# Optimization experiments

Measured on AMD Instinct MI355X. Metric: run time of the kernel, lower is better.

Reference implementation:

```python
import jax, jax.numpy as jnp
import numpy as np

DIM, KEY_DIM, HEADS, RATIO, RES = 384, 32, 8, 4, 7
N = RES * RES
D = RATIO * KEY_DIM          # 128 per-head value dim
DH = D * HEADS               # 1024
NHKD = KEY_DIM * HEADS       # 256
SCALE = KEY_DIM ** -0.5


def _make_bias_idxs(res):
    points = [(i, j) for i in range(res) for j in range(res)]
    offsets = {}
    idxs = []
    for p1 in points:
        for p2 in points:
            off = (abs(p1[0] - p2[0]), abs(p1[1] - p2[1]))
            if off not in offsets:
                offsets[off] = len(offsets)
            idxs.append(offsets[off])
    n = len(points)
    return np.asarray(idxs, dtype=np.int32).reshape(n, n), len(offsets)


def setup_inputs() -> dict:
    key = jax.random.key(0)
    ks = jax.random.split(key, 10)
    B = 2048
    idxs_np, n_off = _make_bias_idxs(RES)
    s = 0.02
    return {
        "x": jax.random.normal(ks[0], (B, N, DIM), jnp.float32),
        "q_w": jax.random.normal(ks[1], (NHKD, DIM), jnp.float32) * s,
        "q_b": jnp.zeros((NHKD,), jnp.float32),
        "k_w": jax.random.normal(ks[2], (NHKD, DIM), jnp.float32) * s,
        "k_b": jnp.zeros((NHKD,), jnp.float32),
        "v_w": jax.random.normal(ks[3], (DH, DIM), jnp.float32) * s,
        "v_b": jnp.zeros((DH,), jnp.float32),
        "proj_w": jax.random.normal(ks[4], (DIM, DH), jnp.float32) * s,
        "proj_b": jnp.zeros((DIM,), jnp.float32),
        "attention_biases": jax.random.normal(ks[5], (HEADS, n_off), jnp.float32) * s,
        "bias_idxs": jnp.asarray(idxs_np),  # [N, N] int32
    }


def reference(x, q_w, q_b, k_w, k_b, v_w, v_b, proj_w, proj_b,
              attention_biases, bias_idxs):
    B, n, _ = x.shape
    q = (x @ q_w.T + q_b).reshape(B, n, HEADS, KEY_DIM)
    k = (x @ k_w.T + k_b).reshape(B, n, HEADS, KEY_DIM)
    v = (x @ v_w.T + v_b).reshape(B, n, HEADS, D)
    # learned relative-position bias gathered per (query, key) pair: [H, N, N]
    ab = attention_biases[:, bias_idxs]
    attn = jnp.einsum("bnhd,bmhd->bhnm", q, k) * SCALE + ab
    attn = jax.nn.softmax(attn, axis=-1)
    out = jnp.einsum("bhnm,bmhd->bnhd", attn, v).reshape(B, n, DH)
    return out @ proj_w.T + proj_b
```

## Files before the change

### kernel.cpp

```cpp
#include <hip/hip_runtime.h>
#include <hip/hip_bf16.h>

#define NTOK   49
#define DIM    384
#define KEY_DIM 32
#define HEADS  8
#define D_HEAD 128
#define SCALE  0.17677669529663687f

typedef short short8 __attribute__((ext_vector_type(8)));
typedef short short4_t __attribute__((ext_vector_type(4)));
typedef float f32x4 __attribute__((ext_vector_type(4)));

__device__ __forceinline__ unsigned short f2bf(float x) {
    union { float f; unsigned u; } v; v.f = x;
    unsigned r = v.u + 0x7fffu + ((v.u >> 16) & 1u);
    return (unsigned short)(r >> 16);
}

__device__ __forceinline__ f32x4 MFMA(short8 a, short8 b, f32x4 c) {
    return __builtin_amdgcn_mfma_f32_16x16x32_bf16(a, b, c, 0, 0, 0);
}

__global__ void prologue(const float* __restrict__ qw, const float* __restrict__ qb,
                         const float* __restrict__ kw,
                         const float* __restrict__ vw, const float* __restrict__ pw,
                         const float* __restrict__ biases, const int* __restrict__ idxs,
                         int n_off,
                         unsigned short* __restrict__ qk_p,
                         unsigned short* __restrict__ vw_p,
                         unsigned short* __restrict__ pw_p,
                         float* __restrict__ qb_s,
                         float* __restrict__ ab_t) {
    int t = blockIdx.x * 256 + threadIdx.x;
    if (t < 24576) {
        int lane = t & 63, kt = (t >> 6) % 12, ntile = t / 768;
        int c = ntile * 16 + (lane & 15), kk = kt * 32 + (lane >> 4) * 8;
        const float* src = (c < 256) ? (qw + c * 384 + kk) : (kw + (c - 256) * 384 + kk);
        float sc = (c < 256) ? SCALE : 1.0f;
        short8 o;
#pragma unroll
        for (int j = 0; j < 8; ++j) o[j] = (short)f2bf(src[j] * sc);
        *(short8*)(qk_p + (size_t)t * 8) = o;
    } else if (t < 73728) {
        int u = t - 24576;
        int lane = u & 63, kt = (u >> 6) % 12, ntile = u / 768;
        int c = ntile * 16 + (lane & 15), kk = kt * 32 + (lane >> 4) * 8;
        const float* src = vw + c * 384 + kk;
        short8 o;
#pragma unroll
        for (int j = 0; j < 8; ++j) o[j] = (short)f2bf(src[j]);
        *(short8*)(vw_p + (size_t)u * 8) = o;
    } else if (t < 122880) {
        int u = t - 73728;
        int lane = u & 63, kt = (u >> 6) % 32, ntile = u / 2048;
        int c = ntile * 16 + (lane & 15), kk = kt * 32 + (lane >> 4) * 8;
        const float* src = pw + c * 1024 + kk;
        short8 o;
#pragma unroll
        for (int j = 0; j < 8; ++j) o[j] = (short)f2bf(src[j]);
        *(short8*)(pw_p + (size_t)u * 8) = o;
    } else if (t < 123136) {
        int u = t - 122880;
        qb_s[u] = qb[u] * SCALE;
    } else if (t < 123136 + 32768) {
        int u = t - 123136;
        int h = u >> 12, n = (u >> 6) & 63, m = u & 63;
        float v = 0.f;
        if (m < 49 && n < 49) v = biases[h * n_off + idxs[n * 49 + m]];
        ab_t[u] = v;
    }
}

__global__ __launch_bounds__(512) void fused_attn(
        const float* __restrict__ x,
        const unsigned short* __restrict__ qkw,
        const unsigned short* __restrict__ vw,
        const unsigned short* __restrict__ pw,
        const float* __restrict__ qb_s, const float* __restrict__ kb,
        const float* __restrict__ vb, const float* __restrict__ pb,
        const float* __restrict__ ab_t,
        float* __restrict__ out) {

    __shared__ __align__(16) unsigned short smem[40656];
    unsigned short* xs  = smem;
    unsigned short* ps  = smem + 19208;
    unsigned short* vsT = smem + 22736;
    unsigned short* qs  = smem + 31952;
    unsigned short* ks2 = smem + 31952 + 2560;
    unsigned short* osA = smem + 31952;

    const int tid  = threadIdx.x;
    const int lane = tid & 63;
    const int wid  = tid >> 6;
    const int l15  = lane & 15;
    const int lg   = lane >> 4;
    const int b    = blockIdx.x;

    const float* xb = x + (size_t)b * (NTOK * DIM);
#pragma unroll 2
    for (int i = tid; i < 4704; i += 512) {
        f32x4 v = __builtin_nontemporal_load(((const f32x4*)xb) + i);
        int f = i * 4;
        int row = f / DIM;
        int col = f - row * DIM;
        short4_t pk;
        pk[0] = (short)f2bf(v[0]); pk[1] = (short)f2bf(v[1]);
        pk[2] = (short)f2bf(v[2]); pk[3] = (short)f2bf(v[3]);
        *(short4_t*)&xs[row * 392 + col] = pk;
    }
    __syncthreads();

    f32x4 pacc[3][4];
#pragma unroll
    for (int i = 0; i < 3; ++i)
#pragma unroll
        for (int j = 0; j < 4; ++j) pacc[i][j] = (f32x4)0.f;

    const f32x4 zf = (f32x4)0.f;

    for (int h = 0; h < HEADS; ++h) {
        {
            const int mh  = wid >> 2;
            const int nt0 = 3 * (wid & 3);
            const int rA0 = min(mh * 32 + l15, 48);
            const int rA1 = min(mh * 32 + 16 + l15, 48);
            f32x4 acc[3][2];
#pragma unroll
            for (int i = 0; i < 3; ++i) { acc[i][0] = zf; acc[i][1] = zf; }

            const short8* bptr[3];
#pragma unroll
            for (int i = 0; i < 3; ++i) {
                int nt = nt0 + i;
                const unsigned short* base; int ntile;
                if (nt < 2)      { base = qkw; ntile = 2 * h + nt; }
                else if (nt < 4) { base = qkw; ntile = 16 + 2 * h + (nt - 2); }
                else             { base = vw;  ntile = 8 * h + (nt - 4); }
                bptr[i] = (const short8*)(base + (size_t)ntile * 12 * 64 * 8);
            }
#pragma unroll
            for (int kt = 0; kt < 12; ++kt) {
                short8 a0 = *(const short8*)&xs[rA0 * 392 + kt * 32 + lg * 8];
                short8 a1 = *(const short8*)&xs[rA1 * 392 + kt * 32 + lg * 8];
#pragma unroll
                for (int i = 0; i < 3; ++i) {
                    short8 bf = bptr[i][kt * 64 + lane];
                    acc[i][0] = MFMA(a0, bf, acc[i][0]);
                    acc[i][1] = MFMA(a1, bf, acc[i][1]);
                }
            }
#pragma unroll
            for (int i = 0; i < 3; ++i) {
                int nt = nt0 + i;
                int c  = nt * 16 + l15;
                if (nt < 4) {
                    int cc = (nt < 2) ? c : c - 32;
                    float bias = (nt < 2) ? qb_s[h * 32 + cc] : kb[h * 32 + cc];
                    unsigned short* dst = (nt < 2) ? qs : ks2;
#pragma unroll
                    for (int j = 0; j < 2; ++j) {
                        int r0 = mh * 32 + j * 16 + lg * 4;
                        f32x4 v = acc[i][j];
#pragma unroll
                        for (int r = 0; r < 4; ++r)
                            dst[(r0 + r) * 40 + cc] = f2bf(v[r] + bias);
                    }
                } else {
                    int d = c - 64;
                    float bias = vb[h * 128 + d];
#pragma unroll
                    for (int j = 0; j < 2; ++j) {
                        int m0 = mh * 32 + j * 16 + lg * 4;
                        f32x4 v = acc[i][j];
                        short4_t pk;
#pragma unroll
                        for (int r = 0; r < 4; ++r) pk[r] = (short)f2bf(v[r] + bias);
                        *(short4_t*)&vsT[d * 72 + m0] = pk;
                    }
                }
            }
        }
        __syncthreads();

        if (wid < 4) {
            const int I = wid;
            const int rq = min(I * 16 + l15, 48);
            short8 bq = *(const short8*)&qs[rq * 40 + lg * 8];
            f32x4 s[4];
#pragma unroll
            for (int J = 0; J < 4; ++J) {
                short8 ak = *(const short8*)&ks2[(J * 16 + l15) * 40 + lg * 8];
                s[J] = MFMA(ak, bq, zf);
            }
            const f32x4* abn = (const f32x4*)(ab_t + ((h * 64 + I * 16 + l15) * 64));
            float sv[16];
            float mx = -1e30f;
#pragma unroll
            for (int J = 0; J < 4; ++J) {
                f32x4 a4 = abn[J * 4 + lg];
#pragma unroll
                for (int r = 0; r < 4; ++r) {
                    int m = J * 16 + lg * 4 + r;
                    float val = s[J][r] + a4[r];
                    if (m >= 49) val = -1e30f;
                    sv[J * 4 + r] = val;
                    mx = fmaxf(mx, val);
                }
            }
            mx = fmaxf(mx, __shfl_xor(mx, 16));
            mx = fmaxf(mx, __shfl_xor(mx, 32));
            float sum = 0.f;
#pragma unroll
            for (int t = 0; t < 16; ++t) { float e = __expf(sv[t] - mx); sv[t] = e; sum += e; }
            sum += __shfl_xor(sum, 16);
            sum += __shfl_xor(sum, 32);
            float inv = 1.0f / sum;
            int n = I * 16 + l15;
            if (n < 49) {
#pragma unroll
                for (int J = 0; J < 4; ++J)
#pragma unroll
                    for (int r = 0; r < 4; ++r) {
                        int m = J * 16 + lg * 4 + r;
                        ps[n * 72 + m] = f2bf(sv[J * 4 + r] * inv);
                    }
            }
        }
        __syncthreads();

        {
            const int np = wid >> 2;
            const int dp = wid & 3;
            const int rp0 = min(np * 32 + l15, 48);
            const int rp1 = min(np * 32 + 16 + l15, 48);
            f32x4 a00 = zf, a01 = zf, a10 = zf, a11 = zf;
#pragma unroll
            for (int kk = 0; kk < 2; ++kk) {
                short8 a0 = *(const short8*)&ps[rp0 * 72 + kk * 32 + lg * 8];
                short8 a1 = *(const short8*)&ps[rp1 * 72 + kk * 32 + lg * 8];
                short8 b0 = *(const short8*)&vsT[(dp * 32 + l15) * 72 + kk * 32 + lg * 8];
                short8 b1 = *(const short8*)&vsT[(dp * 32 + 16 + l15) * 72 + kk * 32 + lg * 8];
                a00 = MFMA(a0, b0, a00); a01 = MFMA(a0, b1, a01);
                a10 = MFMA(a1, b0, a10); a11 = MFMA(a1, b1, a11);
            }
            f32x4 accs[2][2] = {{a00, a01}, {a10, a11}};
#pragma unroll
            for (int jn = 0; jn < 2; ++jn)
#pragma unroll
                for (int jd = 0; jd < 2; ++jd) {
                    int r0 = np * 32 + jn * 16 + lg * 4;
                    int d0 = dp * 32 + jd * 16 + l15;
                    f32x4 v = accs[jn][jd];
#pragma unroll
                    for (int r = 0; r < 4; ++r) osA[(r0 + r) * 136 + d0] = f2bf(v[r]);
                }
        }
        __syncthreads();

        {
            const int nt0 = 3 * wid;
#pragma unroll
            for (int kt = 0; kt < 4; ++kt) {
                short8 a[4];
#pragma unroll
                for (int mi = 0; mi < 4; ++mi)
                    a[mi] = *(const short8*)&osA[(mi * 16 + l15) * 136 + kt * 32 + lg * 8];
#pragma unroll
                for (int i = 0; i < 3; ++i) {
                    short8 bf = ((const short8*)pw)[((size_t)(nt0 + i) * 32 + (h * 4 + kt)) * 64 + lane];
#pragma unroll
                    for (int mi = 0; mi < 4; ++mi)
                        pacc[i][mi] = MFMA(a[mi], bf, pacc[i][mi]);
                }
            }
        }
        __syncthreads();
    }

    float* ob = out + (size_t)b * (NTOK * 384);
#pragma unroll
    for (int i = 0; i < 3; ++i) {
        int c = (3 * wid + i) * 16 + l15;
        float bias = pb[c];
#pragma unroll
        for (int mi = 0; mi < 4; ++mi) {
            f32x4 v = pacc[i][mi];
#pragma unroll
            for (int r = 0; r < 4; ++r) {
                int n = mi * 16 + lg * 4 + r;
                if (n < 49) __builtin_nontemporal_store(v[r] + bias, &ob[n * 384 + c]);
            }
        }
    }
}

extern "C" void kernel_launch(void* const* d_in, const int* in_sizes, int n_in,
                              void* d_out, int out_size, void* d_ws, size_t ws_size,
                              hipStream_t stream) {
    const float* x      = (const float*)d_in[0];
    const float* qw     = (const float*)d_in[1];
    const float* qb     = (const float*)d_in[2];
    const float* kw     = (const float*)d_in[3];
    const float* kb     = (const float*)d_in[4];
    const float* vw     = (const float*)d_in[5];
    const float* vb     = (const float*)d_in[6];
    const float* pw     = (const float*)d_in[7];
    const float* pb     = (const float*)d_in[8];
    const float* biases = (const float*)d_in[9];
    const int*   idxs   = (const int*)d_in[10];
    int n_off = in_sizes[9] / HEADS;

    char* ws = (char*)d_ws;
    unsigned short* qk_p = (unsigned short*)ws;
    unsigned short* vw_p = (unsigned short*)(ws + 393216);
    unsigned short* pw_p = (unsigned short*)(ws + 1179648);
    float*          qb_s = (float*)(ws + 1966080);
    float*          ab_t = (float*)(ws + 1967104);

    prologue<<<609, 256, 0, stream>>>(qw, qb, kw, vw, pw, biases, idxs, n_off,
                                      qk_p, vw_p, pw_p, qb_s, ab_t);
    fused_attn<<<2048, 512, 0, stream>>>(x, qk_p, vw_p, pw_p, qb_s, kb, vb, pb,
                                         ab_t, (float*)d_out);
}
```

Before: 453.6 us.

## Split fused attention into QKV-attention kernel and separate output projection kernel

Splits the single fused kernel into two. attn_qkv computes per-head QKV projections, softmax and P·V, then writes bf16 per-head outputs in MFMA fragment layout to a workspace buffer. out_proj reads them back and applies the projection with a full register accumulator. The aim is to cut LDS use and register pressure so more blocks fit per CU (launch_bounds 512,4). The cost is roughly 268 MB of extra global traffic for the intermediate, and the split only runs when the workspace is large enough.

Result: slower. 478.3 us (+5.4%).

```diff
diff --git a/kernel.cpp b/kernel.cpp
--- a/kernel.cpp
+++ b/kernel.cpp
@@ -72,6 +72,256 @@
     }
 }
 
+__global__ __launch_bounds__(512, 4) void attn_qkv(
+        const float* __restrict__ x,
+        const unsigned short* __restrict__ qkw,
+        const unsigned short* __restrict__ vw,
+        const float* __restrict__ qb_s, const float* __restrict__ kb,
+        const float* __restrict__ vb,
+        const float* __restrict__ ab_t,
+        unsigned short* __restrict__ O_p) {
+
+    __shared__ __align__(16) unsigned short smem[37072];
+    unsigned short* xs  = smem;
+    unsigned short* ps  = smem + 19208;
+    unsigned short* vsT = smem + 22736;
+    unsigned short* qs  = smem + 31952;
+    unsigned short* ks2 = smem + 34512;
+
+    const int tid  = threadIdx.x;
+    const int lane = tid & 63;
+    const int wid  = tid >> 6;
+    const int l15  = lane & 15;
+    const int lg   = lane >> 4;
+    const int b    = blockIdx.x;
+
+    const float* xb = x + (size_t)b * (NTOK * DIM);
+#pragma unroll 2
+    for (int i = tid; i < 4704; i += 512) {
+        f32x4 v = __builtin_nontemporal_load(((const f32x4*)xb) + i);
+        int f = i * 4;
+        int row = f / DIM;
+        int col = f - row * DIM;
+        short4_t pk;
+        pk[0] = (short)f2bf(v[0]); pk[1] = (short)f2bf(v[1]);
+        pk[2] = (short)f2bf(v[2]); pk[3] = (short)f2bf(v[3]);
+        *(short4_t*)&xs[row * 392 + col] = pk;
+    }
+    __syncthreads();
+
+    const f32x4 zf = (f32x4)0.f;
+
+    for (int h = 0; h < HEADS; ++h) {
+        {
+            const int mh  = wid >> 2;
+            const int nt0 = 3 * (wid & 3);
+            const int rA0 = min(mh * 32 + l15, 48);
+            const int rA1 = min(mh * 32 + 16 + l15, 48);
+            f32x4 acc[3][2];
+#pragma unroll
+            for (int i = 0; i < 3; ++i) { acc[i][0] = zf; acc[i][1] = zf; }
+
+            const short8* bptr[3];
+#pragma unroll
+            for (int i = 0; i < 3; ++i) {
+                int nt = nt0 + i;
+                const unsigned short* base; int ntile;
+                if (nt < 2)      { base = qkw; ntile = 2 * h + nt; }
+                else if (nt < 4) { base = qkw; ntile = 16 + 2 * h + (nt - 2); }
+                else             { base = vw;  ntile = 8 * h + (nt - 4); }
+                bptr[i] = (const short8*)(base + (size_t)ntile * 12 * 64 * 8);
+            }
+#pragma unroll
+            for (int kt = 0; kt < 12; ++kt) {
+                short8 a0 = *(const short8*)&xs[rA0 * 392 + kt * 32 + lg * 8];
+                short8 a1 = *(const short8*)&xs[rA1 * 392 + kt * 32 + lg * 8];
+#pragma unroll
+                for (int i = 0; i < 3; ++i) {
+                    short8 bf = bptr[i][kt * 64 + lane];
+                    acc[i][0] = MFMA(a0, bf, acc[i][0]);
+                    acc[i][1] = MFMA(a1, bf, acc[i][1]);
+                }
+            }
+#pragma unroll
+            for (int i = 0; i < 3; ++i) {
+                int nt = nt0 + i;
+                int c  = nt * 16 + l15;
+                if (nt < 4) {
+                    int cc = (nt < 2) ? c : c - 32;
+                    float bias = (nt < 2) ? qb_s[h * 32 + cc] : kb[h * 32 + cc];
+                    unsigned short* dst = (nt < 2) ? qs : ks2;
+#pragma unroll
+                    for (int j = 0; j < 2; ++j) {
+                        int r0 = mh * 32 + j * 16 + lg * 4;
+                        f32x4 v = acc[i][j];
+#pragma unroll
+                        for (int r = 0; r < 4; ++r)
+                            dst[(r0 + r) * 40 + cc] = f2bf(v[r] + bias);
+                    }
+                } else {
+                    int d = c - 64;
+                    float bias = vb[h * 128 + d];
+#pragma unroll
+                    for (int j = 0; j < 2; ++j) {
+                        int m0 = mh * 32 + j * 16 + lg * 4;
+                        f32x4 v = acc[i][j];
+                        short4_t pk;
+#pragma unroll
+                        for (int r = 0; r < 4; ++r) pk[r] = (short)f2bf(v[r] + bias);
+                        *(short4_t*)&vsT[d * 72 + m0] = pk;
+                    }
+                }
+            }
+        }
+        __syncthreads();
+
+        if (wid < 4) {
+            const int I = wid;
+            const int rq = min(I * 16 + l15, 48);
+            short8 bq = *(const short8*)&qs[rq * 40 + lg * 8];
+            f32x4 s[4];
+#pragma unroll
+            for (int J = 0; J < 4; ++J) {
+                short8 ak = *(const short8*)&ks2[(J * 16 + l15) * 40 + lg * 8];
+                s[J] = MFMA(ak, bq, zf);
+            }
+            const f32x4* abn = (const f32x4*)(ab_t + ((h * 64 + I * 16 + l15) * 64));
+            float sv[16];
+            float mx = -1e30f;
+#pragma unroll
+            for (int J = 0; J < 4; ++J) {
+                f32x4 a4 = abn[J * 4 + lg];
+#pragma unroll
+                for (int r = 0; r < 4; ++r) {
+                    int m = J * 16 + lg * 4 + r;
+                    float val = s[J][r] + a4[r];
+                    if (m >= 49) val = -1e30f;
+                    sv[J * 4 + r] = val;
+                    mx = fmaxf(mx, val);
+                }
+            }
+            mx = fmaxf(mx, __shfl_xor(mx, 16));
+            mx = fmaxf(mx, __shfl_xor(mx, 32));
+            float sum = 0.f;
+#pragma unroll
+            for (int t = 0; t < 16; ++t) { float e = __expf(sv[t] - mx); sv[t] = e; sum += e; }
+            sum += __shfl_xor(sum, 16);
+            sum += __shfl_xor(sum, 32);
+            float inv = 1.0f / sum;
+            int n = I * 16 + l15;
+            if (n < 49) {
+#pragma unroll
+                for (int J = 0; J < 4; ++J)
+#pragma unroll
+                    for (int r = 0; r < 4; ++r) {
+                        int m = J * 16 + lg * 4 + r;
+                        ps[n * 72 + m] = f2bf(sv[J * 4 + r] * inv);
+                    }
+            }
+        }
+        __syncthreads();
+
+        {
+            const int np = wid >> 2;
+            const int dp = wid & 3;
+            const int rp0 = min(np * 32 + l15, 48);
+            const int rp1 = min(np * 32 + 16 + l15, 48);
+            f32x4 a00 = zf, a01 = zf, a10 = zf, a11 = zf;
+#pragma unroll
+            for (int kk = 0; kk < 2; ++kk) {
+                short8 a0 = *(const short8*)&ps[rp0 * 72 + kk * 32 + lg * 8];
+                short8 a1 = *(const short8*)&ps[rp1 * 72 + kk * 32 + lg * 8];
+                short8 b0 = *(const short8*)&vsT[(dp * 32 + l15) * 72 + kk * 32 + lg * 8];
+                short8 b1 = *(const short8*)&vsT[(dp * 32 + 16 + l15) * 72 + kk * 32 + lg * 8];
+                a00 = MFMA(a0, b0, a00); a01 = MFMA(a0, b1, a01);
+                a10 = MFMA(a1, b0, a10); a11 = MFMA(a1, b1, a11);
+            }
+            f32x4 accs[2][2] = {{a00, a01}, {a10, a11}};
+            unsigned short* ob = O_p + (((size_t)b * 8 + h) * 32) * 256;
+#pragma unroll
+            for (int jn = 0; jn < 2; ++jn)
+#pragma unroll
+                for (int jd = 0; jd < 2; ++jd) {
+                    int frag = (np * 2 + jn) * 8 + (dp * 2 + jd);
+                    f32x4 v = accs[jn][jd];
+                    short4_t pk;
+#pragma unroll
+                    for (int r = 0; r < 4; ++r) pk[r] = (short)f2bf(v[r]);
+                    __builtin_nontemporal_store(pk, (short4_t*)(ob + frag * 256 + lane * 4));
+                }
+        }
+        __syncthreads();
+    }
+}
+
+__global__ __launch_bounds__(256) void out_proj(
+        const unsigned short* __restrict__ O_p,
+        const unsigned short* __restrict__ pw,
+        const float* __restrict__ pb,
+        float* __restrict__ out) {
+
+    __shared__ __align__(16) unsigned short osB[64 * 136];
+
+    const int tid  = threadIdx.x;
+    const int lane = tid & 63;
+    const int wid  = tid >> 6;
+    const int l15  = lane & 15;
+    const int lg   = lane >> 4;
+    const int b    = blockIdx.x;
+
+    f32x4 acc[6][4];
+#pragma unroll
+    for (int i = 0; i < 6; ++i)
+#pragma unroll
+        for (int j = 0; j < 4; ++j) acc[i][j] = (f32x4)0.f;
+
+    for (int h = 0; h < HEADS; ++h) {
+        const unsigned short* ob = O_p + (((size_t)b * 8 + h) * 32) * 256;
+#pragma unroll
+        for (int s = tid; s < 2048; s += 256) {
+            int frag = s >> 6, ln = s & 63;
+            short4_t v = __builtin_nontemporal_load((const short4_t*)(ob + frag * 256 + ln * 4));
+            int mt = frag >> 3, dt = frag & 7;
+            int r0 = mt * 16 + ((ln >> 4) << 2), c = dt * 16 + (ln & 15);
+#pragma unroll
+            for (int r = 0; r < 4; ++r) osB[(r0 + r) * 136 + c] = v[r];
+        }
+        __syncthreads();
+
+#pragma unroll
+        for (int kt = 0; kt < 4; ++kt) {
+            short8 a[4];
+#pragma unroll
+            for (int mt = 0; mt < 4; ++mt)
+                a[mt] = *(const short8*)&osB[(mt * 16 + l15) * 136 + kt * 32 + lg * 8];
+#pragma unroll
+            for (int i = 0; i < 6; ++i) {
+                short8 bf = ((const short8*)pw)[((size_t)(wid * 6 + i) * 32 + (h * 4 + kt)) * 64 + lane];
+#pragma unroll
+                for (int mt = 0; mt < 4; ++mt)
+                    acc[i][mt] = MFMA(a[mt], bf, acc[i][mt]);
+            }
+        }
+        __syncthreads();
+    }
+
+    float* obase = out + (size_t)b * (NTOK * 384);
+#pragma unroll
+    for (int i = 0; i < 6; ++i) {
+        int c = (wid * 6 + i) * 16 + l15;
+        float bias = pb[c];
+#pragma unroll
+        for (int mt = 0; mt < 4; ++mt) {
+            f32x4 v = acc[i][mt];
+#pragma unroll
+            for (int r = 0; r < 4; ++r) {
+                int n = mt * 16 + lg * 4 + r;
+                if (n < 49) __builtin_nontemporal_store(v[r] + bias, &obase[n * 384 + c]);
+            }
+        }
+    }
+}
+
 __global__ __launch_bounds__(512) void fused_attn(
         const float* __restrict__ x,
         const unsigned short* __restrict__ qkw,
@@ -317,9 +567,17 @@
     unsigned short* pw_p = (unsigned short*)(ws + 1179648);
     float*          qb_s = (float*)(ws + 1966080);
     float*          ab_t = (float*)(ws + 1967104);
+    unsigned short* O_p  = (unsigned short*)(ws + 2098176);
+
+    const size_t need = 2098176ull + (size_t)2048 * 8 * 32 * 256 * 2;
 
     prologue<<<609, 256, 0, stream>>>(qw, qb, kw, vw, pw, biases, idxs, n_off,
                                       qk_p, vw_p, pw_p, qb_s, ab_t);
-    fused_attn<<<2048, 512, 0, stream>>>(x, qk_p, vw_p, pw_p, qb_s, kb, vb, pb,
-                                         ab_t, (float*)d_out);
-}
+    if (ws_size >= need) {
+        attn_qkv<<<2048, 512, 0, stream>>>(x, qk_p, vw_p, qb_s, kb, vb, ab_t, O_p);
+        out_proj<<<2048, 256, 0, stream>>>(O_p, pw_p, pb, (float*)d_out);
+    } else {
+        fused_attn<<<2048, 512, 0, stream>>>(x, qk_p, vw_p, pw_p, qb_s, kb, vb, pb,
+                                             ab_t, (float*)d_out);
+    }
+}
```
